# Optimization experiments

Measured on AMD Instinct MI355X. Metric: run time of the kernel, lower is better.

## Reference

```python
import jax, jax.numpy as jnp
import numpy as np

H = 12       # heads
D = 768      # hidden size
DH = D // H  # head dim = 64
SCALE = 1.0 / jnp.sqrt(jnp.float32(DH))
LN_EPS = 1e-3  # keras LayerNormalization default epsilon


def setup_inputs() -> dict:
    key = jax.random.key(0)
    ks = jax.random.split(key, 8)
    B, L = 16, 512
    s = 0.02  # truncated-normal-ish init scale
    return {
        "x": jax.random.normal(ks[0], (B, L, D), jnp.float32),
        "mask": jnp.ones((B, L), jnp.int32),
        "Wq": jax.random.normal(ks[1], (D, D), jnp.float32) * s,
        "bq": jnp.zeros((D,), jnp.float32),
        "Wk": jax.random.normal(ks[2], (D, D), jnp.float32) * s,
        "bk": jnp.zeros((D,), jnp.float32),
        "Wv": jax.random.normal(ks[3], (D, D), jnp.float32) * s,
        "bv": jnp.zeros((D,), jnp.float32),
        "Wo": jax.random.normal(ks[4], (D, D), jnp.float32) * s,
        "bo": jnp.zeros((D,), jnp.float32),
        "gamma": jnp.ones((D,), jnp.float32),
        "beta": jnp.zeros((D,), jnp.float32),
    }


def reference(x, mask, Wq, bq, Wk, bk, Wv, bv, Wo, bo, gamma, beta):
    B, L, _ = x.shape
    # QKV projections, split into heads: [B, L, H, DH]
    q = (x @ Wq + bq).reshape(B, L, H, DH)
    k = (x @ Wk + bk).reshape(B, L, H, DH)
    v = (x @ Wv + bv).reshape(B, L, H, DH)
    # scaled dot-product scores: [B, H, Lq, Lk]
    scores = jnp.einsum('bqhd,bkhd->bhqk', q, k) * SCALE
    # key-side padding mask (mask==0 -> -inf)
    neg = jnp.float32(-1e9)
    scores = jnp.where(mask[:, None, None, :] > 0, scores, neg)
    p = jax.nn.softmax(scores, axis=-1)
    # dropout rate fixed to 0.0 -> identity
    ctx = jnp.einsum('bhqk,bkhd->bqhd', p, v).reshape(B, L, D)
    attn_out = ctx @ Wo + bo
    # residual + LayerNorm (keras default eps=1e-3)
    y = x + attn_out
    mu = jnp.mean(y, axis=-1, keepdims=True)
    var = jnp.mean(jnp.square(y - mu), axis=-1, keepdims=True)
    return gamma * (y - mu) * jax.lax.rsqrt(var + LN_EPS) + beta
```

## Files before the change

kernel.cpp:

```cpp
#include <hip/hip_runtime.h>
#include <math.h>

#define NH 12
#define DMODEL 768
#define DHEAD 64
#define BATCH 16
#define SEQ 512
#define NTOK (BATCH*SEQ)
#define ATTN_SCALE 0.125f
#define LN_EPS 1e-3f
#define PADP 72
#define NKT 12

typedef __attribute__((ext_vector_type(8))) short  bf16x8;
typedef __attribute__((ext_vector_type(4))) float  f32x4;

__device__ __forceinline__ unsigned short f2bf(float f) {
    unsigned int u = __float_as_uint(f);
    unsigned int r = (u + 0x7fffu + ((u >> 16) & 1u)) >> 16;
    return (unsigned short)r;
}

__device__ __forceinline__ void async_copy16(const void* g, void* l) {
    __builtin_amdgcn_global_load_lds((const __attribute__((address_space(1))) void*)g,
                                     (__attribute__((address_space(3))) void*)l,
                                     16, 0, 0);
}

__global__ __launch_bounds__(256) void prep_kernel(
    const float* __restrict__ x,
    const float* __restrict__ Wq, const float* __restrict__ Wk,
    const float* __restrict__ Wv, const float* __restrict__ Wo,
    unsigned short* __restrict__ xb,
    unsigned short* __restrict__ tq, unsigned short* __restrict__ tk,
    unsigned short* __restrict__ tv, unsigned short* __restrict__ to_)
{
    __shared__ float tile[32][33];
    const int bid = blockIdx.x;
    const int tid = threadIdx.x;

    if (bid < 6144) {
        int i = (bid * 256 + tid) * 4;
        const float4 v = *(const float4*)(x + i);
        unsigned long long pack =
              (unsigned long long)f2bf(v.x)
            | ((unsigned long long)f2bf(v.y) << 16)
            | ((unsigned long long)f2bf(v.z) << 32)
            | ((unsigned long long)f2bf(v.w) << 48);
        *(unsigned long long*)(xb + i) = pack;
        return;
    }

    const int t   = bid - 6144;
    const int zz  = t / 576;
    const int rem = t % 576;
    const float* W = (zz == 0) ? Wq : (zz == 1) ? Wk : (zz == 2) ? Wv : Wo;
    unsigned short* T = (zz == 0) ? tq : (zz == 1) ? tk : (zz == 2) ? tv : to_;

    const int bx = (rem / 24) * 32;
    const int by = (rem % 24) * 32;
    const int tx = tid & 31, ty = tid >> 5;

    #pragma unroll
    for (int i = 0; i < 32; i += 8)
        tile[ty + i][tx] = W[(size_t)(bx + ty + i) * DMODEL + by + tx];
    __syncthreads();
    #pragma unroll
    for (int i = 0; i < 32; i += 8)
        T[(size_t)(by + ty + i) * DMODEL + bx + tx] = f2bf(tile[tx][ty + i]);
}

#define SBAR() do { \
    __builtin_amdgcn_sched_barrier(0); \
    __builtin_amdgcn_s_barrier(); \
    __builtin_amdgcn_sched_barrier(0); \
} while (0)

#define VMWAIT0() do { \
    __builtin_amdgcn_sched_barrier(0); \
    asm volatile("s_waitcnt vmcnt(0)" ::: "memory"); \
    __builtin_amdgcn_sched_barrier(0); \
} while (0)

#define QSTAGE(kt, buf) do { \
    const int _k0 = (kt) * 64; \
    _Pragma("unroll") \
    for (int _i = 0; _i < 4; ++_i) \
        async_copy16(aSrc + (size_t)_i * (8 * DMODEL) + _k0, &As[buf][(w * 4 + _i) * 512]); \
    _Pragma("unroll") \
    for (int _i = 0; _i < 4; ++_i) \
        async_copy16(bSrc + (size_t)_i * (64 * DMODEL) + _k0, &Bs[buf][(w + 8 * _i) * 512]); \
    if (w < 4) \
        async_copy16(bSrc + (size_t)4 * (64 * DMODEL) + _k0, &Bs[buf][(w + 32) * 512]); \
} while (0)

#define QLDA(buf) do { \
    _Pragma("unroll") \
    for (int _m = 0; _m < 4; ++_m) { \
        const int _row = wm * 64 + _m * 16 + l16; \
        aF[_m][0] = *(const bf16x8*)&As[buf][_row * 64 + p0]; \
        aF[_m][1] = *(const bf16x8*)&As[buf][_row * 64 + (p0 ^ 32)]; \
    } } while (0)

#define QLDB(buf, nh) do { \
    _Pragma("unroll") \
    for (int _n = 0; _n < 3; ++_n) { \
        const int _row = wn * 144 + ((nh) * 3 + _n) * 16 + l16; \
        bF[_n][0] = *(const bf16x8*)&Bs[buf][_row * 64 + p0]; \
        bF[_n][1] = *(const bf16x8*)&Bs[buf][_row * 64 + (p0 ^ 32)]; \
    } } while (0)

#define QMM(nh) do { \
    __builtin_amdgcn_s_setprio(1); \
    _Pragma("unroll") \
    for (int _k = 0; _k < 2; ++_k) \
      _Pragma("unroll") \
      for (int _m = 0; _m < 4; ++_m) \
        _Pragma("unroll") \
        for (int _n = 0; _n < 3; ++_n) \
          acc[_m][(nh) * 3 + _n] = __builtin_amdgcn_mfma_f32_16x16x32_bf16( \
              aF[_m][_k], bF[_n][_k], acc[_m][(nh) * 3 + _n], 0, 0, 0); \
    __builtin_amdgcn_s_setprio(0); \
} while (0)

#define QTILE(t, c, o, hasNext) do { \
    if (hasNext) QSTAGE((t) + 1, o); \
    QLDA(c); \
    QLDB(c, 0); \
    QMM(0); \
    SBAR(); \
    QLDB(c, 1); \
    QMM(1); \
    SBAR(); \
    QLDB(c, 2); \
    QMM(2); \
    if (hasNext) VMWAIT0(); \
    SBAR(); \
} while (0)

__global__ __launch_bounds__(512, 2) void gemm8p_qkv(
    const unsigned short* __restrict__ xb, const unsigned short* __restrict__ wt,
    const float* __restrict__ bq, const float* __restrict__ bk, const float* __restrict__ bv,
    unsigned short* __restrict__ o0, unsigned short* __restrict__ o1,
    unsigned short* __restrict__ o2)
{
    __shared__ __align__(16) unsigned short As[2][256 * 64];
    __shared__ __align__(16) unsigned short Bs[2][288 * 64];

    const int orig = blockIdx.x;
    const int wg   = (orig & 7) * 32 + (orig >> 3);
    const int m0   = (wg >> 3) * 256;
    const int n0   = (wg & 7) * 288;

    const int tid  = threadIdx.x;
    const int lane = tid & 63;
    const int w    = tid >> 6;
    const int wm   = w >> 1, wn = w & 1;
    const int quad = lane >> 4;
    const int l16  = lane & 15;
    const int rloc = lane >> 3;
    const int csw  = (lane & 7) ^ rloc;
    const int p0   = (quad ^ (l16 & 7)) * 8;

    const unsigned short* aSrc = xb + (size_t)(m0 + w * 32 + rloc) * DMODEL + csw * 8;
    const unsigned short* bSrc = wt + (size_t)(n0 + w * 8  + rloc) * DMODEL + csw * 8;

    f32x4 acc[4][9] = {};
    bf16x8 aF[4][2], bF[3][2];

    QSTAGE(0, 0);
    VMWAIT0();
    SBAR();

    #pragma unroll 1
    for (int tt = 0; tt < NKT / 2; ++tt) {
        QTILE(2 * tt,     0, 1, 1);
        QTILE(2 * tt + 1, 1, 0, (tt < NKT / 2 - 1));
    }

    #pragma unroll
    for (int nf = 0; nf < 9; ++nf) {
        const int ncg = n0 + wn * 144 + nf * 16 + l16;
        const int zz  = (ncg >= 1536) ? 2 : (ncg >= 768) ? 1 : 0;
        const int ncl = ncg - zz * 768;
        const int h = ncl >> 6, dh = ncl & 63;
        const float bval = ((zz == 0) ? bq : (zz == 1) ? bk : bv)[ncl];
        if (zz == 2) {
            #pragma unroll
            for (int mi = 0; mi < 4; ++mi) {
                const int mbase = m0 + wm * 64 + mi * 16 + quad * 4;
                const int bi = mbase >> 9, l = mbase & 511;
                unsigned long long pack = 0;
                #pragma unroll
                for (int r = 0; r < 4; ++r)
                    pack |= (unsigned long long)f2bf(acc[mi][nf][r] + bval) << (16 * r);
                *(unsigned long long*)(o2 + ((size_t)((bi * NH + h) * DHEAD + dh)) * SEQ + l) = pack;
            }
        } else {
            const float sc = (zz == 0) ? ATTN_SCALE : 1.0f;
            unsigned short* out = (zz == 0) ? o0 : o1;
            #pragma unroll
            for (int mi = 0; mi < 4; ++mi) {
                const int mbase = m0 + wm * 64 + mi * 16 + quad * 4;
                #pragma unroll
                for (int r = 0; r < 4; ++r) {
                    const int t = mbase + r;
                    const int bi = t >> 9, l = t & 511;
                    out[(size_t)((bi * NH + h) * SEQ + l) * DHEAD + dh] =
                        f2bf((acc[mi][nf][r] + bval) * sc);
                }
            }
        }
    }
}

__global__ __launch_bounds__(256, 4) void mfma_gemm_oproj(
    const unsigned short* __restrict__ ctxb, const unsigned short* __restrict__ wto,
    const float* __restrict__ bo, const float* __restrict__ x,
    float* __restrict__ y)
{
    __shared__ __align__(16) unsigned short As[128 * 64];
    __shared__ __align__(16) unsigned short Bs[128 * 64];

    const int tid  = threadIdx.x;
    const int lane = tid & 63;
    const int w    = tid >> 6;
    const int wm   = w >> 1, wn = w & 1;
    const int m0   = blockIdx.x * 128;
    const int n0   = blockIdx.y * 128;
    const int quad = lane >> 4;
    const int l16  = lane & 15;

    const int rloc = lane >> 3;
    const int csw  = (lane & 7) ^ rloc;
    int rowS[4];
    #pragma unroll
    for (int ii = 0; ii < 4; ++ii) rowS[ii] = (4 * w + ii) * 8 + rloc;
    const int p0 = ((quad ^ (l16 & 7)) * 8);

    f32x4 acc[4][4] = {};

    for (int kb = 0; kb < NKT; ++kb) {
        const int k0 = kb * 64;
        #pragma unroll
        for (int ii = 0; ii < 4; ++ii) {
            async_copy16(ctxb + (size_t)(m0 + rowS[ii]) * DMODEL + k0 + csw * 8,
                         As + (4 * w + ii) * 512);
            async_copy16(wto  + (size_t)(n0 + rowS[ii]) * DMODEL + k0 + csw * 8,
                         Bs + (4 * w + ii) * 512);
        }
        __syncthreads();

        #pragma unroll
        for (int ks = 0; ks < 2; ++ks) {
            const int po = p0 ^ (ks * 32);
            bf16x8 a[4], b[4];
            #pragma unroll
            for (int mi = 0; mi < 4; ++mi)
                a[mi] = *(const bf16x8*)&As[(wm * 64 + mi * 16 + l16) * 64 + po];
            #pragma unroll
            for (int ni = 0; ni < 4; ++ni)
                b[ni] = *(const bf16x8*)&Bs[(wn * 64 + ni * 16 + l16) * 64 + po];
            #pragma unroll
            for (int mi = 0; mi < 4; ++mi)
                #pragma unroll
                for (int ni = 0; ni < 4; ++ni)
                    acc[mi][ni] = __builtin_amdgcn_mfma_f32_16x16x32_bf16(a[mi], b[ni], acc[mi][ni], 0, 0, 0);
        }
        __syncthreads();
    }

    #pragma unroll
    for (int ni = 0; ni < 4; ++ni) {
        const int ncol = n0 + wn * 64 + ni * 16 + l16;
        const float bv_ = bo[ncol];
        #pragma unroll
        for (int mi = 0; mi < 4; ++mi) {
            const int mbase = m0 + wm * 64 + mi * 16 + quad * 4;
            #pragma unroll
            for (int r = 0; r < 4; ++r) {
                const size_t idx = (size_t)(mbase + r) * DMODEL + ncol;
                y[idx] = acc[mi][ni][r] + bv_ + x[idx];
            }
        }
    }
}

__global__ __launch_bounds__(256) void attn_mfma_kernel(
    const unsigned short* __restrict__ q, const unsigned short* __restrict__ k,
    const unsigned short* __restrict__ vt, const int* __restrict__ mask,
    unsigned short* __restrict__ ctxb)
{
    __shared__ __align__(16) unsigned short Qs[64 * 64];
    __shared__ __align__(16) unsigned short Ks[2][64 * 64];
    __shared__ __align__(16) unsigned short Vs[2][64 * 64];
    __shared__ __align__(16) unsigned short Ps[64 * PADP];
    __shared__ float maskV[SEQ];
    __shared__ int   cleanS[8];

    const int tid  = threadIdx.x;
    const int lane = tid & 63;
    const int w    = tid >> 6;
    const int quad = lane >> 4;
    const int l16  = lane & 15;

    const int id = blockIdx.x;
    const int qt = id / (BATCH * NH);
    const int g  = id % (BATCH * NH);
    const int b  = g / NH, h = g % NH;
    const int q0 = qt * 64;

    const unsigned short* qp  = q  + ((size_t)(b * NH + h) * SEQ + q0) * DHEAD;
    const unsigned short* kp  = k  + (size_t)(b * NH + h) * SEQ * DHEAD;
    const unsigned short* vtp = vt + (size_t)(b * NH + h) * DHEAD * SEQ;

    const int rloc = lane >> 3;
    const int csw  = (lane & 7) ^ rloc;
    const int p0   = (quad ^ (l16 & 7)) * 8;

    #pragma unroll
    for (int ii = 0; ii < 2; ++ii) {
        const int inst = 2 * w + ii;
        async_copy16(qp  + (size_t)(inst * 8 + rloc) * DHEAD + csw * 8, Qs + inst * 512);
        async_copy16(kp  + (size_t)(inst * 8 + rloc) * DHEAD + csw * 8, &Ks[0][inst * 512]);
        async_copy16(vtp + (size_t)(inst * 8 + rloc) * SEQ + csw * 8,   &Vs[0][inst * 512]);
    }
    #pragma unroll
    for (int j = 0; j < 2; ++j) {
        const int idx = tid + 256 * j;
        const bool pm = mask[b * SEQ + idx] > 0;
        maskV[idx] = pm ? 0.f : -1e9f;
        const unsigned long long bb = __ballot(pm);
        if (lane == 0) cleanS[w + 4 * j] = (bb == ~0ull) ? 1 : 0;
    }
    __syncthreads();

    bf16x8 aQ[2];
    #pragma unroll
    for (int ks = 0; ks < 2; ++ks)
        aQ[ks] = *(const bf16x8*)&Qs[(w * 16 + l16) * 64 + (p0 ^ (ks * 32))];

    bf16x8 ones;
    #pragma unroll
    for (int j = 0; j < 8; ++j) ones[j] = (short)0x3F80;

    f32x4 o[4] = {};
    f32x4 lsum = {0.f, 0.f, 0.f, 0.f};
    const f32x4 zf = {0.f, 0.f, 0.f, 0.f};

    #pragma unroll
    for (int it = 0; it < 8; ++it) {
        const int cur = it & 1;
        if (it + 1 < 8) {
            const int kt1 = (it + 1) * 64;
            #pragma unroll
            for (int ii = 0; ii < 2; ++ii) {
                const int inst = 2 * w + ii;
                async_copy16(kp  + (size_t)(kt1 + inst * 8 + rloc) * DHEAD + csw * 8,
                             &Ks[1 - cur][inst * 512]);
                async_copy16(vtp + (size_t)(inst * 8 + rloc) * SEQ + kt1 + csw * 8,
                             &Vs[1 - cur][inst * 512]);
            }
        }
        const int kt = it * 64;

        f32x4 s[4];
        #pragma unroll
        for (int ni = 0; ni < 4; ++ni) {
            bf16x8 bK0 = *(const bf16x8*)&Ks[cur][(ni * 16 + l16) * 64 + p0];
            bf16x8 bK1 = *(const bf16x8*)&Ks[cur][(ni * 16 + l16) * 64 + (p0 ^ 32)];
            f32x4 t0 = __builtin_amdgcn_mfma_f32_16x16x32_bf16(aQ[0], bK0, zf, 0, 0, 0);
            s[ni] = __builtin_amdgcn_mfma_f32_16x16x32_bf16(aQ[1], bK1, t0, 0, 0, 0);
        }
        if (cleanS[it] == 0) {
            #pragma unroll
            for (int ni = 0; ni < 4; ++ni) {
                const float mk = maskV[kt + ni * 16 + l16];
                #pragma unroll
                for (int r = 0; r < 4; ++r) s[ni][r] += mk;
            }
        }

        #pragma unroll
        for (int ni = 0; ni < 4; ++ni)
            #pragma unroll
            for (int r = 0; r < 4; ++r)
                Ps[(w * 16 + quad * 4 + r) * PADP + ni * 16 + l16]
                    = (unsigned short)(__float_as_uint(__expf(s[ni][r])) >> 16);

        bf16x8 aP[2];
        #pragma unroll
        for (int ks = 0; ks < 2; ++ks)
            aP[ks] = *(const bf16x8*)&Ps[(w * 16 + l16) * PADP + quad * 8 + ks * 32];

        lsum = __builtin_amdgcn_mfma_f32_16x16x32_bf16(aP[0], ones, lsum, 0, 0, 0);
        lsum = __builtin_amdgcn_mfma_f32_16x16x32_bf16(aP[1], ones, lsum, 0, 0, 0);

        #pragma unroll
        for (int ni = 0; ni < 4; ++ni) {
            bf16x8 bV0 = *(const bf16x8*)&Vs[cur][(ni * 16 + l16) * 64 + p0];
            bf16x8 bV1 = *(const bf16x8*)&Vs[cur][(ni * 16 + l16) * 64 + (p0 ^ 32)];
            o[ni] = __builtin_amdgcn_mfma_f32_16x16x32_bf16(aP[0], bV0, o[ni], 0, 0, 0);
            o[ni] = __builtin_amdgcn_mfma_f32_16x16x32_bf16(aP[1], bV1, o[ni], 0, 0, 0);
        }

        __syncthreads();
    }

    #pragma unroll
    for (int r = 0; r < 4; ++r) {
        const float inv = 1.f / lsum[r];
        const int tok = q0 + w * 16 + quad * 4 + r;
        #pragma unroll
        for (int ni = 0; ni < 4; ++ni)
            ctxb[(size_t)(b * SEQ + tok) * DMODEL + h * DHEAD + ni * 16 + l16]
                = f2bf(o[ni][r] * inv);
    }
}

__global__ __launch_bounds__(256) void ln_kernel(
    const float* __restrict__ y, const float* __restrict__ gamma,
    const float* __restrict__ beta, float* __restrict__ out)
{
    const int t   = blockIdx.x;
    const int tid = threadIdx.x;
    const float* row = y + (size_t)t * DMODEL;

    float vals[3];
    float s = 0.f, s2 = 0.f;
    #pragma unroll
    for (int i = 0; i < 3; ++i) {
        float vv = row[tid + 256 * i];
        vals[i] = vv;
        s  += vv;
        s2 += vv * vv;
    }
    #pragma unroll
    for (int off = 32; off > 0; off >>= 1) {
        s  += __shfl_down(s,  off);
        s2 += __shfl_down(s2, off);
    }
    __shared__ float rbuf[8];
    int w = tid >> 6;
    if ((tid & 63) == 0) { rbuf[w] = s; rbuf[4 + w] = s2; }
    __syncthreads();
    float ts  = rbuf[0] + rbuf[1] + rbuf[2] + rbuf[3];
    float ts2 = rbuf[4] + rbuf[5] + rbuf[6] + rbuf[7];
    float mu  = ts * (1.f / DMODEL);
    float var = ts2 * (1.f / DMODEL) - mu * mu;
    float inv = rsqrtf(var + LN_EPS);
    #pragma unroll
    for (int i = 0; i < 3; ++i) {
        int c = tid + 256 * i;
        out[(size_t)t * DMODEL + c] = gamma[c] * (vals[i] - mu) * inv + beta[c];
    }
}

extern "C" void kernel_launch(void* const* d_in, const int* in_sizes, int n_in,
                              void* d_out, int out_size, void* d_ws, size_t ws_size,
                              hipStream_t stream) {
    const float* x     = (const float*)d_in[0];
    const int*   mask  = (const int*)  d_in[1];
    const float* Wq    = (const float*)d_in[2];
    const float* bq    = (const float*)d_in[3];
    const float* Wk    = (const float*)d_in[4];
    const float* bk    = (const float*)d_in[5];
    const float* Wv    = (const float*)d_in[6];
    const float* bv    = (const float*)d_in[7];
    const float* Wo    = (const float*)d_in[8];
    const float* bo    = (const float*)d_in[9];
    const float* gamma = (const float*)d_in[10];
    const float* beta  = (const float*)d_in[11];
    float* out = (float*)d_out;

    const size_t perTok = (size_t)NTOK * DMODEL;
    const size_t perW   = (size_t)DMODEL * DMODEL;

    unsigned short* xb   = (unsigned short*)d_ws;
    unsigned short* wtq  = xb + perTok;
    unsigned short* wtk  = wtq + perW;
    unsigned short* wtv  = wtk + perW;
    unsigned short* wto  = wtv + perW;
    unsigned short* qb   = wto + perW;
    unsigned short* kb   = qb + perTok;
    unsigned short* vb   = kb + perTok;
    unsigned short* ctxb = vb + perTok;
    float* y = out;

    prep_kernel<<<6144 + 2304, 256, 0, stream>>>(
        x, Wq, Wk, Wv, Wo, xb, wtq, wtk, wtv, wto);

    gemm8p_qkv<<<256, 512, 0, stream>>>(xb, wtq, bq, bk, bv, qb, kb, vb);

    attn_mfma_kernel<<<dim3((SEQ / 64) * BATCH * NH), 256, 0, stream>>>(
        qb, kb, vb, mask, ctxb);

    mfma_gemm_oproj<<<dim3(NTOK / 128, DMODEL / 128), 256, 0, stream>>>(
        ctxb, wto, bo, x, y);

    ln_kernel<<<NTOK, 256, 0, stream>>>(y, gamma, beta, out);
}
```

Baseline: 202.3 us.

## Triple-buffer QKV and output-projection GEMMs with K-step 32 async pipelines

Replaces the double-buffered K=64 QKV GEMM and the unpipelined output-projection GEMM with triple-buffered K=32 pipelines that prefetch two stages ahead and use partial vmcnt waits. The output projection is retiled to 128x192 tiles with 512-thread blocks and a grouped block order. The goal is to hide global-load latency and cut barrier stalls. In exchange it drops the XOR LDS swizzle, which risks bank conflicts, and it uses more barriers per K step.

```diff
diff --git a/kernel.cpp b/kernel.cpp
--- a/kernel.cpp
+++ b/kernel.cpp
@@ -10,7 +10,7 @@
 #define ATTN_SCALE 0.125f
 #define LN_EPS 1e-3f
 #define PADP 72
-#define NKT 12
+#define NST 24
 
 typedef __attribute__((ext_vector_type(8))) short  bf16x8;
 typedef __attribute__((ext_vector_type(4))) float  f32x4;
@@ -26,6 +26,18 @@
                                      (__attribute__((address_space(3))) void*)l,
                                      16, 0, 0);
 }
+
+#define SBAR() do { \
+    __builtin_amdgcn_sched_barrier(0); \
+    __builtin_amdgcn_s_barrier(); \
+    __builtin_amdgcn_sched_barrier(0); \
+} while (0)
+
+#define VMW(n) do { \
+    __builtin_amdgcn_sched_barrier(0); \
+    asm volatile("s_waitcnt vmcnt(" #n ")" ::: "memory"); \
+    __builtin_amdgcn_sched_barrier(0); \
+} while (0)
 
 __global__ __launch_bounds__(256) void prep_kernel(
     const float* __restrict__ x,
@@ -70,82 +82,46 @@
         T[(size_t)(by + ty + i) * DMODEL + bx + tx] = f2bf(tile[tx][ty + i]);
 }
 
-#define SBAR() do { \
-    __builtin_amdgcn_sched_barrier(0); \
-    __builtin_amdgcn_s_barrier(); \
-    __builtin_amdgcn_sched_barrier(0); \
-} while (0)
-
-#define VMWAIT0() do { \
-    __builtin_amdgcn_sched_barrier(0); \
-    asm volatile("s_waitcnt vmcnt(0)" ::: "memory"); \
-    __builtin_amdgcn_sched_barrier(0); \
-} while (0)
-
-#define QSTAGE(kt, buf) do { \
-    const int _k0 = (kt) * 64; \
-    _Pragma("unroll") \
-    for (int _i = 0; _i < 4; ++_i) \
-        async_copy16(aSrc + (size_t)_i * (8 * DMODEL) + _k0, &As[buf][(w * 4 + _i) * 512]); \
-    _Pragma("unroll") \
-    for (int _i = 0; _i < 4; ++_i) \
-        async_copy16(bSrc + (size_t)_i * (64 * DMODEL) + _k0, &Bs[buf][(w + 8 * _i) * 512]); \
-    if (w < 4) \
-        async_copy16(bSrc + (size_t)4 * (64 * DMODEL) + _k0, &Bs[buf][(w + 32) * 512]); \
-} while (0)
-
-#define QLDA(buf) do { \
-    _Pragma("unroll") \
-    for (int _m = 0; _m < 4; ++_m) { \
-        const int _row = wm * 64 + _m * 16 + l16; \
-        aF[_m][0] = *(const bf16x8*)&As[buf][_row * 64 + p0]; \
-        aF[_m][1] = *(const bf16x8*)&As[buf][_row * 64 + (p0 ^ 32)]; \
-    } } while (0)
-
-#define QLDB(buf, nh) do { \
-    _Pragma("unroll") \
-    for (int _n = 0; _n < 3; ++_n) { \
-        const int _row = wn * 144 + ((nh) * 3 + _n) * 16 + l16; \
-        bF[_n][0] = *(const bf16x8*)&Bs[buf][_row * 64 + p0]; \
-        bF[_n][1] = *(const bf16x8*)&Bs[buf][_row * 64 + (p0 ^ 32)]; \
-    } } while (0)
-
-#define QMM(nh) do { \
+#define QSTAGE(kt, sb) do { \
+    const int _k0 = (kt) * 32; \
+    async_copy16(aS + _k0,                    &As[sb][(2 * w)     * 512]); \
+    async_copy16(aS + 16 * DMODEL + _k0,      &As[sb][(2 * w + 1) * 512]); \
+    async_copy16(bS + _k0,                    &Bs[sb][(2 * w)     * 512]); \
+    async_copy16(bS + 16 * DMODEL + _k0,      &Bs[sb][(2 * w + 1) * 512]); \
+    if (w < 2) \
+        async_copy16(bS2 + _k0,               &Bs[sb][(16 + w)    * 512]); \
+} while (0)
+
+#define QSTEP(stepIdx, bc, sb) do { \
+    const int _st = (stepIdx); \
+    if (_st + 2 < NST) QSTAGE(_st + 2, sb); \
+    bf16x8 aF[4], bF[9]; \
+    _Pragma("unroll") \
+    for (int _m = 0; _m < 4; ++_m) \
+        aF[_m] = *(const bf16x8*)&As[bc][(wm * 64 + _m * 16 + l16) * 32 + quad * 8]; \
+    _Pragma("unroll") \
+    for (int _n = 0; _n < 9; ++_n) \
+        bF[_n] = *(const bf16x8*)&Bs[bc][(wn * 144 + _n * 16 + l16) * 32 + quad * 8]; \
     __builtin_amdgcn_s_setprio(1); \
     _Pragma("unroll") \
-    for (int _k = 0; _k < 2; ++_k) \
+    for (int _n = 0; _n < 9; ++_n) \
       _Pragma("unroll") \
       for (int _m = 0; _m < 4; ++_m) \
-        _Pragma("unroll") \
-        for (int _n = 0; _n < 3; ++_n) \
-          acc[_m][(nh) * 3 + _n] = __builtin_amdgcn_mfma_f32_16x16x32_bf16( \
-              aF[_m][_k], bF[_n][_k], acc[_m][(nh) * 3 + _n], 0, 0, 0); \
+        acc[_m][_n] = __builtin_amdgcn_mfma_f32_16x16x32_bf16(aF[_m], bF[_n], acc[_m][_n], 0, 0, 0); \
     __builtin_amdgcn_s_setprio(0); \
-} while (0)
-
-#define QTILE(t, c, o, hasNext) do { \
-    if (hasNext) QSTAGE((t) + 1, o); \
-    QLDA(c); \
-    QLDB(c, 0); \
-    QMM(0); \
-    SBAR(); \
-    QLDB(c, 1); \
-    QMM(1); \
-    SBAR(); \
-    QLDB(c, 2); \
-    QMM(2); \
-    if (hasNext) VMWAIT0(); \
-    SBAR(); \
-} while (0)
-
-__global__ __launch_bounds__(512, 2) void gemm8p_qkv(
+    if (_st <= NST - 3)      { if (w < 2) VMW(5); else VMW(4); } \
+    else if (_st == NST - 2) VMW(0); \
+    if (_st < NST - 1) SBAR(); \
+} while (0)
+
+__global__ __launch_bounds__(512, 2) void gemm_tri_qkv(
     const unsigned short* __restrict__ xb, const unsigned short* __restrict__ wt,
     const float* __restrict__ bq, const float* __restrict__ bk, const float* __restrict__ bv,
     unsigned short* __restrict__ o0, unsigned short* __restrict__ o1,
     unsigned short* __restrict__ o2)
 {
-    __shared__ __align__(16) unsigned short As[2][256 * 64];
-    __shared__ __align__(16) unsigned short Bs[2][288 * 64];
+    __shared__ __align__(16) unsigned short As[3][256 * 32];
+    __shared__ __align__(16) unsigned short Bs[3][288 * 32];
 
     const int orig = blockIdx.x;
     const int wg   = (orig & 7) * 32 + (orig >> 3);
@@ -158,24 +134,25 @@
     const int wm   = w >> 1, wn = w & 1;
     const int quad = lane >> 4;
     const int l16  = lane & 15;
-    const int rloc = lane >> 3;
-    const int csw  = (lane & 7) ^ rloc;
-    const int p0   = (quad ^ (l16 & 7)) * 8;
-
-    const unsigned short* aSrc = xb + (size_t)(m0 + w * 32 + rloc) * DMODEL + csw * 8;
-    const unsigned short* bSrc = wt + (size_t)(n0 + w * 8  + rloc) * DMODEL + csw * 8;
+    const int lr   = lane >> 2;
+    const int lc   = (lane & 3) * 8;
+
+    const unsigned short* aS  = xb + (size_t)(m0 + 32 * w + lr) * DMODEL + lc;
+    const unsigned short* bS  = wt + (size_t)(n0 + 32 * w + lr) * DMODEL + lc;
+    const unsigned short* bS2 = wt + (size_t)(n0 + 256 + 16 * w + lr) * DMODEL + lc;
 
     f32x4 acc[4][9] = {};
-    bf16x8 aF[4][2], bF[3][2];
 
     QSTAGE(0, 0);
-    VMWAIT0();
+    QSTAGE(1, 1);
+    if (w < 2) VMW(5); else VMW(4);
     SBAR();
 
     #pragma unroll 1
-    for (int tt = 0; tt < NKT / 2; ++tt) {
-        QTILE(2 * tt,     0, 1, 1);
-        QTILE(2 * tt + 1, 1, 0, (tt < NKT / 2 - 1));
+    for (int tt = 0; tt < NST / 3; ++tt) {
+        QSTEP(3 * tt + 0, 0, 2);
+        QSTEP(3 * tt + 1, 1, 0);
+        QSTEP(3 * tt + 2, 2, 1);
     }
 
     #pragma unroll
@@ -214,65 +191,79 @@
     }
 }
 
-__global__ __launch_bounds__(256, 4) void mfma_gemm_oproj(
+#define OSTAGE(kt, sb) do { \
+    const int _k0 = (kt) * 32; \
+    async_copy16(aS + _k0,  &Ao[sb][w * 512]); \
+    async_copy16(bS + _k0,  &Bo[sb][w * 512]); \
+    if (w < 4) \
+        async_copy16(bS2 + _k0, &Bo[sb][(8 + w) * 512]); \
+} while (0)
+
+#define OSTEP(stepIdx, bc, sb) do { \
+    const int _st = (stepIdx); \
+    if (_st + 2 < NST) OSTAGE(_st + 2, sb); \
+    bf16x8 aF[4], bF[3]; \
+    _Pragma("unroll") \
+    for (int _m = 0; _m < 4; ++_m) \
+        aF[_m] = *(const bf16x8*)&Ao[bc][(wm * 64 + _m * 16 + l16) * 32 + quad * 8]; \
+    _Pragma("unroll") \
+    for (int _n = 0; _n < 3; ++_n) \
+        bF[_n] = *(const bf16x8*)&Bo[bc][(wn * 48 + _n * 16 + l16) * 32 + quad * 8]; \
+    __builtin_amdgcn_s_setprio(1); \
+    _Pragma("unroll") \
+    for (int _n = 0; _n < 3; ++_n) \
+      _Pragma("unroll") \
+      for (int _m = 0; _m < 4; ++_m) \
+        acc[_m][_n] = __builtin_amdgcn_mfma_f32_16x16x32_bf16(aF[_m], bF[_n], acc[_m][_n], 0, 0, 0); \
+    __builtin_amdgcn_s_setprio(0); \
+    if (_st <= NST - 3)      { if (w < 4) VMW(3); else VMW(2); } \
+    else if (_st == NST - 2) VMW(0); \
+    if (_st < NST - 1) SBAR(); \
+} while (0)
+
+__global__ __launch_bounds__(512, 2) void gemm_tri_oproj(
     const unsigned short* __restrict__ ctxb, const unsigned short* __restrict__ wto,
     const float* __restrict__ bo, const float* __restrict__ x,
     float* __restrict__ y)
 {
-    __shared__ __align__(16) unsigned short As[128 * 64];
-    __shared__ __align__(16) unsigned short Bs[128 * 64];
+    __shared__ __align__(16) unsigned short Ao[3][128 * 32];
+    __shared__ __align__(16) unsigned short Bo[3][192 * 32];
+
+    const int orig = blockIdx.x;
+    const int wg   = (orig & 7) * 32 + (orig >> 3);
+    const int m0   = (wg >> 2) * 128;
+    const int n0   = (wg & 3) * 192;
 
     const int tid  = threadIdx.x;
     const int lane = tid & 63;
     const int w    = tid >> 6;
-    const int wm   = w >> 1, wn = w & 1;
-    const int m0   = blockIdx.x * 128;
-    const int n0   = blockIdx.y * 128;
+    const int wm   = w >> 2, wn = w & 3;
     const int quad = lane >> 4;
     const int l16  = lane & 15;
-
-    const int rloc = lane >> 3;
-    const int csw  = (lane & 7) ^ rloc;
-    int rowS[4];
-    #pragma unroll
-    for (int ii = 0; ii < 4; ++ii) rowS[ii] = (4 * w + ii) * 8 + rloc;
-    const int p0 = ((quad ^ (l16 & 7)) * 8);
-
-    f32x4 acc[4][4] = {};
-
-    for (int kb = 0; kb < NKT; ++kb) {
-        const int k0 = kb * 64;
-        #pragma unroll
-        for (int ii = 0; ii < 4; ++ii) {
-            async_copy16(ctxb + (size_t)(m0 + rowS[ii]) * DMODEL + k0 + csw * 8,
-                         As + (4 * w + ii) * 512);
-            async_copy16(wto  + (size_t)(n0 + rowS[ii]) * DMODEL + k0 + csw * 8,
-                         Bs + (4 * w + ii) * 512);
-        }
-        __syncthreads();
-
-        #pragma unroll
-        for (int ks = 0; ks < 2; ++ks) {
-            const int po = p0 ^ (ks * 32);
-            bf16x8 a[4], b[4];
-            #pragma unroll
-            for (int mi = 0; mi < 4; ++mi)
-                a[mi] = *(const bf16x8*)&As[(wm * 64 + mi * 16 + l16) * 64 + po];
-            #pragma unroll
-            for (int ni = 0; ni < 4; ++ni)
-                b[ni] = *(const bf16x8*)&Bs[(wn * 64 + ni * 16 + l16) * 64 + po];
-            #pragma unroll
-            for (int mi = 0; mi < 4; ++mi)
-                #pragma unroll
-                for (int ni = 0; ni < 4; ++ni)
-                    acc[mi][ni] = __builtin_amdgcn_mfma_f32_16x16x32_bf16(a[mi], b[ni], acc[mi][ni], 0, 0, 0);
-        }
-        __syncthreads();
-    }
-
-    #pragma unroll
-    for (int ni = 0; ni < 4; ++ni) {
-        const int ncol = n0 + wn * 64 + ni * 16 + l16;
+    const int lr   = lane >> 2;
+    const int lc   = (lane & 3) * 8;
+
+    const unsigned short* aS  = ctxb + (size_t)(m0 + 16 * w + lr) * DMODEL + lc;
+    const unsigned short* bS  = wto  + (size_t)(n0 + 16 * w + lr) * DMODEL + lc;
+    const unsigned short* bS2 = wto  + (size_t)(n0 + 128 + 16 * w + lr) * DMODEL + lc;
+
+    f32x4 acc[4][3] = {};
+
+    OSTAGE(0, 0);
+    OSTAGE(1, 1);
+    if (w < 4) VMW(3); else VMW(2);
+    SBAR();
+
+    #pragma unroll 1
+    for (int tt = 0; tt < NST / 3; ++tt) {
+        OSTEP(3 * tt + 0, 0, 2);
+        OSTEP(3 * tt + 1, 1, 0);
+        OSTEP(3 * tt + 2, 2, 1);
+    }
+
+    #pragma unroll
+    for (int ni = 0; ni < 3; ++ni) {
+        const int ncol = n0 + wn * 48 + ni * 16 + l16;
         const float bv_ = bo[ncol];
         #pragma unroll
         for (int mi = 0; mi < 4; ++mi) {
@@ -490,13 +481,12 @@
     prep_kernel<<<6144 + 2304, 256, 0, stream>>>(
         x, Wq, Wk, Wv, Wo, xb, wtq, wtk, wtv, wto);
 
-    gemm8p_qkv<<<256, 512, 0, stream>>>(xb, wtq, bq, bk, bv, qb, kb, vb);
+    gemm_tri_qkv<<<256, 512, 0, stream>>>(xb, wtq, bq, bk, bv, qb, kb, vb);
 
     attn_mfma_kernel<<<dim3((SEQ / 64) * BATCH * NH), 256, 0, stream>>>(
         qb, kb, vb, mask, ctxb);
 
-    mfma_gemm_oproj<<<dim3(NTOK / 128, DMODEL / 128), 256, 0, stream>>>(
-        ctxb, wto, bo, x, y);
+    gemm_tri_oproj<<<256, 512, 0, stream>>>(ctxb, wto, bo, x, y);
 
     ln_kernel<<<NTOK, 256, 0, stream>>>(y, gamma, beta, out);
 }
```

Result: slower. 213.0 us (+5.3%).

## Double-buffer output projection GEMM with async LDS staging and 128x192 tiles

Applied to the files above, without the earlier changes.

Rewrites the output-projection GEMM to use 512-thread blocks with 128x192 tiles, double-buffered LDS staging via global_load_lds, an XCD-aware block swizzle over 256 blocks, and an 8-wave 2x4 layout. It replaces the old single-buffer loop, which synchronised twice per k-step and could not overlap loads with MFMA. The QKV GEMM macros are restructured so that B-fragment loads are scoped per sub-tile, and the intermediate barriers inside each tile are removed. LDS use rises, and a launch grid of 256 blocks may underfill the device.

```diff
diff --git a/kernel.cpp b/kernel.cpp
--- a/kernel.cpp
+++ b/kernel.cpp
@@ -26,6 +26,18 @@
                                      (__attribute__((address_space(3))) void*)l,
                                      16, 0, 0);
 }
+
+#define SBAR() do { \
+    __builtin_amdgcn_sched_barrier(0); \
+    __builtin_amdgcn_s_barrier(); \
+    __builtin_amdgcn_sched_barrier(0); \
+} while (0)
+
+#define VMW0() do { \
+    __builtin_amdgcn_sched_barrier(0); \
+    asm volatile("s_waitcnt vmcnt(0)" ::: "memory"); \
+    __builtin_amdgcn_sched_barrier(0); \
+} while (0)
 
 __global__ __launch_bounds__(256) void prep_kernel(
     const float* __restrict__ x,
@@ -70,75 +82,52 @@
         T[(size_t)(by + ty + i) * DMODEL + bx + tx] = f2bf(tile[tx][ty + i]);
 }
 
-#define SBAR() do { \
-    __builtin_amdgcn_sched_barrier(0); \
-    __builtin_amdgcn_s_barrier(); \
-    __builtin_amdgcn_sched_barrier(0); \
+#define QSTAGE(kt, sb) do { \
+    const int _k0 = (kt) * 64; \
+    _Pragma("unroll") \
+    for (int _i = 0; _i < 4; ++_i) \
+        async_copy16(aSrc + (size_t)_i * (8 * DMODEL) + _k0, &As[sb][(w * 4 + _i) * 512]); \
+    _Pragma("unroll") \
+    for (int _i = 0; _i < 4; ++_i) \
+        async_copy16(bSrc + (size_t)_i * (64 * DMODEL) + _k0, &Bs[sb][(w + 8 * _i) * 512]); \
+    if (w < 4) \
+        async_copy16(bSrc + (size_t)4 * (64 * DMODEL) + _k0, &Bs[sb][(w + 32) * 512]); \
 } while (0)
 
-#define VMWAIT0() do { \
-    __builtin_amdgcn_sched_barrier(0); \
-    asm volatile("s_waitcnt vmcnt(0)" ::: "memory"); \
-    __builtin_amdgcn_sched_barrier(0); \
-} while (0)
-
-#define QSTAGE(kt, buf) do { \
-    const int _k0 = (kt) * 64; \
-    _Pragma("unroll") \
-    for (int _i = 0; _i < 4; ++_i) \
-        async_copy16(aSrc + (size_t)_i * (8 * DMODEL) + _k0, &As[buf][(w * 4 + _i) * 512]); \
-    _Pragma("unroll") \
-    for (int _i = 0; _i < 4; ++_i) \
-        async_copy16(bSrc + (size_t)_i * (64 * DMODEL) + _k0, &Bs[buf][(w + 8 * _i) * 512]); \
-    if (w < 4) \
-        async_copy16(bSrc + (size_t)4 * (64 * DMODEL) + _k0, &Bs[buf][(w + 32) * 512]); \
-} while (0)
-
-#define QLDA(buf) do { \
+#define QTILE(t, c, o, hasNext) do { \
+    if (hasNext) QSTAGE((t) + 1, o); \
+    bf16x8 aF[4][2]; \
     _Pragma("unroll") \
     for (int _m = 0; _m < 4; ++_m) { \
         const int _row = wm * 64 + _m * 16 + l16; \
-        aF[_m][0] = *(const bf16x8*)&As[buf][_row * 64 + p0]; \
-        aF[_m][1] = *(const bf16x8*)&As[buf][_row * 64 + (p0 ^ 32)]; \
-    } } while (0)
-
-#define QLDB(buf, nh) do { \
-    _Pragma("unroll") \
-    for (int _n = 0; _n < 3; ++_n) { \
-        const int _row = wn * 144 + ((nh) * 3 + _n) * 16 + l16; \
-        bF[_n][0] = *(const bf16x8*)&Bs[buf][_row * 64 + p0]; \
-        bF[_n][1] = *(const bf16x8*)&Bs[buf][_row * 64 + (p0 ^ 32)]; \
-    } } while (0)
-
-#define QMM(nh) do { \
-    __builtin_amdgcn_s_setprio(1); \
-    _Pragma("unroll") \
-    for (int _k = 0; _k < 2; ++_k) \
-      _Pragma("unroll") \
-      for (int _m = 0; _m < 4; ++_m) \
+        aF[_m][0] = *(const bf16x8*)&As[c][_row * 64 + p0]; \
+        aF[_m][1] = *(const bf16x8*)&As[c][_row * 64 + (p0 ^ 32)]; \
+    } \
+    _Pragma("unroll") \
+    for (int _nh = 0; _nh < 3; ++_nh) { \
+        bf16x8 bF[3][2]; \
         _Pragma("unroll") \
-        for (int _n = 0; _n < 3; ++_n) \
-          acc[_m][(nh) * 3 + _n] = __builtin_amdgcn_mfma_f32_16x16x32_bf16( \
-              aF[_m][_k], bF[_n][_k], acc[_m][(nh) * 3 + _n], 0, 0, 0); \
-    __builtin_amdgcn_s_setprio(0); \
-} while (0)
-
-#define QTILE(t, c, o, hasNext) do { \
-    if (hasNext) QSTAGE((t) + 1, o); \
-    QLDA(c); \
-    QLDB(c, 0); \
-    QMM(0); \
-    SBAR(); \
-    QLDB(c, 1); \
-    QMM(1); \
-    SBAR(); \
-    QLDB(c, 2); \
-    QMM(2); \
-    if (hasNext) VMWAIT0(); \
+        for (int _n = 0; _n < 3; ++_n) { \
+            const int _row = wn * 144 + (_nh * 3 + _n) * 16 + l16; \
+            bF[_n][0] = *(const bf16x8*)&Bs[c][_row * 64 + p0]; \
+            bF[_n][1] = *(const bf16x8*)&Bs[c][_row * 64 + (p0 ^ 32)]; \
+        } \
+        __builtin_amdgcn_s_setprio(1); \
+        _Pragma("unroll") \
+        for (int _k = 0; _k < 2; ++_k) \
+          _Pragma("unroll") \
+          for (int _m = 0; _m < 4; ++_m) \
+            _Pragma("unroll") \
+            for (int _n = 0; _n < 3; ++_n) \
+              acc[_m][_nh * 3 + _n] = __builtin_amdgcn_mfma_f32_16x16x32_bf16( \
+                  aF[_m][_k], bF[_n][_k], acc[_m][_nh * 3 + _n], 0, 0, 0); \
+        __builtin_amdgcn_s_setprio(0); \
+    } \
+    if (hasNext) VMW0(); \
     SBAR(); \
 } while (0)
 
-__global__ __launch_bounds__(512, 2) void gemm8p_qkv(
+__global__ __launch_bounds__(512, 2) void gemm_db_qkv(
     const unsigned short* __restrict__ xb, const unsigned short* __restrict__ wt,
     const float* __restrict__ bq, const float* __restrict__ bk, const float* __restrict__ bv,
     unsigned short* __restrict__ o0, unsigned short* __restrict__ o1,
@@ -166,10 +155,9 @@
     const unsigned short* bSrc = wt + (size_t)(n0 + w * 8  + rloc) * DMODEL + csw * 8;
 
     f32x4 acc[4][9] = {};
-    bf16x8 aF[4][2], bF[3][2];
 
     QSTAGE(0, 0);
-    VMWAIT0();
+    VMW0();
     SBAR();
 
     #pragma unroll 1
@@ -214,65 +202,86 @@
     }
 }
 
-__global__ __launch_bounds__(256, 4) void mfma_gemm_oproj(
+#define OSTAGE(kt, sb) do { \
+    const int _k0 = (kt) * 64; \
+    _Pragma("unroll") \
+    for (int _i = 0; _i < 2; ++_i) \
+        async_copy16(aSrc + (size_t)_i * (8 * DMODEL) + _k0, &Ao[sb][(w * 2 + _i) * 512]); \
+    _Pragma("unroll") \
+    for (int _i = 0; _i < 3; ++_i) \
+        async_copy16(bSrc + (size_t)_i * (8 * DMODEL) + _k0, &Bo[sb][(w * 3 + _i) * 512]); \
+} while (0)
+
+#define OTILE(t, c, o, hasNext) do { \
+    if (hasNext) OSTAGE((t) + 1, o); \
+    bf16x8 aF[4][2], bF[3][2]; \
+    _Pragma("unroll") \
+    for (int _m = 0; _m < 4; ++_m) { \
+        const int _row = wm * 64 + _m * 16 + l16; \
+        aF[_m][0] = *(const bf16x8*)&Ao[c][_row * 64 + p0]; \
+        aF[_m][1] = *(const bf16x8*)&Ao[c][_row * 64 + (p0 ^ 32)]; \
+    } \
+    _Pragma("unroll") \
+    for (int _n = 0; _n < 3; ++_n) { \
+        const int _row = wn * 48 + _n * 16 + l16; \
+        bF[_n][0] = *(const bf16x8*)&Bo[c][_row * 64 + p0]; \
+        bF[_n][1] = *(const bf16x8*)&Bo[c][_row * 64 + (p0 ^ 32)]; \
+    } \
+    __builtin_amdgcn_s_setprio(1); \
+    _Pragma("unroll") \
+    for (int _k = 0; _k < 2; ++_k) \
+      _Pragma("unroll") \
+      for (int _m = 0; _m < 4; ++_m) \
+        _Pragma("unroll") \
+        for (int _n = 0; _n < 3; ++_n) \
+          acc[_m][_n] = __builtin_amdgcn_mfma_f32_16x16x32_bf16( \
+              aF[_m][_k], bF[_n][_k], acc[_m][_n], 0, 0, 0); \
+    __builtin_amdgcn_s_setprio(0); \
+    if (hasNext) VMW0(); \
+    SBAR(); \
+} while (0)
+
+__global__ __launch_bounds__(512, 2) void gemm_db_oproj(
     const unsigned short* __restrict__ ctxb, const unsigned short* __restrict__ wto,
     const float* __restrict__ bo, const float* __restrict__ x,
     float* __restrict__ y)
 {
-    __shared__ __align__(16) unsigned short As[128 * 64];
-    __shared__ __align__(16) unsigned short Bs[128 * 64];
+    __shared__ __align__(16) unsigned short Ao[2][132 * 64];
+    __shared__ __align__(16) unsigned short Bo[2][192 * 64];
+
+    const int orig = blockIdx.x;
+    const int wg   = (orig & 7) * 32 + (orig >> 3);
+    const int m0   = (wg >> 2) * 128;
+    const int n0   = (wg & 3) * 192;
 
     const int tid  = threadIdx.x;
     const int lane = tid & 63;
     const int w    = tid >> 6;
-    const int wm   = w >> 1, wn = w & 1;
-    const int m0   = blockIdx.x * 128;
-    const int n0   = blockIdx.y * 128;
+    const int wm   = w >> 2, wn = w & 3;
     const int quad = lane >> 4;
     const int l16  = lane & 15;
-
     const int rloc = lane >> 3;
     const int csw  = (lane & 7) ^ rloc;
-    int rowS[4];
-    #pragma unroll
-    for (int ii = 0; ii < 4; ++ii) rowS[ii] = (4 * w + ii) * 8 + rloc;
-    const int p0 = ((quad ^ (l16 & 7)) * 8);
-
-    f32x4 acc[4][4] = {};
-
-    for (int kb = 0; kb < NKT; ++kb) {
-        const int k0 = kb * 64;
-        #pragma unroll
-        for (int ii = 0; ii < 4; ++ii) {
-            async_copy16(ctxb + (size_t)(m0 + rowS[ii]) * DMODEL + k0 + csw * 8,
-                         As + (4 * w + ii) * 512);
-            async_copy16(wto  + (size_t)(n0 + rowS[ii]) * DMODEL + k0 + csw * 8,
-                         Bs + (4 * w + ii) * 512);
-        }
-        __syncthreads();
-
-        #pragma unroll
-        for (int ks = 0; ks < 2; ++ks) {
-            const int po = p0 ^ (ks * 32);
-            bf16x8 a[4], b[4];
-            #pragma unroll
-            for (int mi = 0; mi < 4; ++mi)
-                a[mi] = *(const bf16x8*)&As[(wm * 64 + mi * 16 + l16) * 64 + po];
-            #pragma unroll
-            for (int ni = 0; ni < 4; ++ni)
-                b[ni] = *(const bf16x8*)&Bs[(wn * 64 + ni * 16 + l16) * 64 + po];
-            #pragma unroll
-            for (int mi = 0; mi < 4; ++mi)
-                #pragma unroll
-                for (int ni = 0; ni < 4; ++ni)
-                    acc[mi][ni] = __builtin_amdgcn_mfma_f32_16x16x32_bf16(a[mi], b[ni], acc[mi][ni], 0, 0, 0);
-        }
-        __syncthreads();
-    }
-
-    #pragma unroll
-    for (int ni = 0; ni < 4; ++ni) {
-        const int ncol = n0 + wn * 64 + ni * 16 + l16;
+    const int p0   = (quad ^ (l16 & 7)) * 8;
+
+    const unsigned short* aSrc = ctxb + (size_t)(m0 + w * 16 + rloc) * DMODEL + csw * 8;
+    const unsigned short* bSrc = wto  + (size_t)(n0 + w * 24 + rloc) * DMODEL + csw * 8;
+
+    f32x4 acc[4][3] = {};
+
+    OSTAGE(0, 0);
+    VMW0();
+    SBAR();
+
+    #pragma unroll 1
+    for (int tt = 0; tt < NKT / 2; ++tt) {
+        OTILE(2 * tt,     0, 1, 1);
+        OTILE(2 * tt + 1, 1, 0, (tt < NKT / 2 - 1));
+    }
+
+    #pragma unroll
+    for (int ni = 0; ni < 3; ++ni) {
+        const int ncol = n0 + wn * 48 + ni * 16 + l16;
         const float bv_ = bo[ncol];
         #pragma unroll
         for (int mi = 0; mi < 4; ++mi) {
@@ -490,13 +499,12 @@
     prep_kernel<<<6144 + 2304, 256, 0, stream>>>(
         x, Wq, Wk, Wv, Wo, xb, wtq, wtk, wtv, wto);
 
-    gemm8p_qkv<<<256, 512, 0, stream>>>(xb, wtq, bq, bk, bv, qb, kb, vb);
+    gemm_db_qkv<<<256, 512, 0, stream>>>(xb, wtq, bq, bk, bv, qb, kb, vb);
 
     attn_mfma_kernel<<<dim3((SEQ / 64) * BATCH * NH), 256, 0, stream>>>(
         qb, kb, vb, mask, ctxb);
 
-    mfma_gemm_oproj<<<dim3(NTOK / 128, DMODEL / 128), 256, 0, stream>>>(
-        ctxb, wto, bo, x, y);
+    gemm_db_oproj<<<256, 512, 0, stream>>>(ctxb, wto, bo, x, y);
 
     ln_kernel<<<NTOK, 256, 0, stream>>>(y, gamma, beta, out);
 }
```

Result: faster. 194.4 us (-3.9%).
